# Kernel optimization log

Measured on AMD Instinct MI355X. Metric: run time of the kernel, lower is better.

Reference implementation:

```python
import jax, jax.numpy as jnp
import numpy as np

N_TICKS = 550
N_PMTS = 12
SI = 47  # SiPM grid is 47x47 = 2209
BIN_SIGMA = 0.1
GAUSS_NORM = 1.0 / (BIN_SIGMA * 2.5066282746)


def _dense_init(k, fan_in, fan_out):
    lim = float(np.sqrt(6.0 / (fan_in + fan_out)))  # glorot_uniform (keras Dense default)
    W = jax.random.uniform(k, (fan_in, fan_out), jnp.float32, -lim, lim)
    b = jnp.zeros((fan_out,), jnp.float32)
    return W, b


def setup_inputs() -> dict:
    key = jax.random.key(0)
    ks = jax.random.split(key, 10)
    B, N = 4, 8192  # events x electrons-per-event (ragged list densified)
    xy = jax.random.normal(ks[0], (B, N, 2), jnp.float32)
    z = jax.random.uniform(ks[1], (B, N, 1), jnp.float32, minval=0.0, maxval=549.0)
    electrons = jnp.concatenate([xy, z], axis=-1)  # [B, N, 3] = (x, y, z_ticks)
    weight = jax.random.uniform(ks[2], (B, N), jnp.float32)  # lifetime survival weight
    Wp1, bp1 = _dense_init(ks[3], 2, 28)
    Wp2, bp2 = _dense_init(ks[4], 28, N_PMTS)
    Ws1, bs1 = _dense_init(ks[5], 2, 64)
    Ws2, bs2 = _dense_init(ks[6], 64, 128)
    Ws3, bs3 = _dense_init(ks[7], 128, 256)
    Ws4, bs4 = _dense_init(ks[8], 256, SI * SI)
    pmt_scale = jnp.ones((N_PMTS,), jnp.float32)
    si_scale = jnp.ones((SI * SI,), jnp.float32)
    return dict(electrons=electrons, weight=weight,
                Wp1=Wp1, bp1=bp1, Wp2=Wp2, bp2=bp2, pmt_scale=pmt_scale,
                Ws1=Ws1, bs1=bs1, Ws2=Ws2, bs2=bs2, Ws3=Ws3, bs3=bs3,
                Ws4=Ws4, bs4=bs4, si_scale=si_scale)


def reference(electrons, weight, Wp1, bp1, Wp2, bp2, pmt_scale,
              Ws1, bs1, Ws2, bs2, Ws3, bs3, Ws4, bs4, si_scale):
    B = electrons.shape[0]
    xy = electrons[..., 0:2]            # [B, N, 2]
    z = electrons[..., 2]               # [B, N] in tick units
    # tf.linspace(0.5, n_ticks-0.5, 550) == bin centers
    ticks = jnp.arange(N_TICKS, dtype=electrons.dtype) + 0.5  # [T]
    # per-electron Gaussian over time ticks, scaled by lifetime weight: [B, N, T]
    exp_values = (GAUSS_NORM
                  * jnp.exp(-(ticks - z[..., None]) ** 2 / BIN_SIGMA)
                  * weight[..., None])
    # PMT response MLP: 2 -> 28 -> 12, sigmoid activations
    h = jax.nn.sigmoid(xy @ Wp1 + bp1)
    pmt_resp = jax.nn.sigmoid(h @ Wp2 + bp2) * pmt_scale ** 2    # [B, N, 12]
    # sparse(hist)^T @ response, then transpose -> [B, 12, T]
    pmt_result = jnp.einsum('bnt,bnp->bpt', exp_values, pmt_resp)
    # SiPM response MLP: 2 -> 64 -> 128 -> 256 -> 2209, sigmoid activations
    s = jax.nn.sigmoid(xy @ Ws1 + bs1)
    s = jax.nn.sigmoid(s @ Ws2 + bs2)
    s = jax.nn.sigmoid(s @ Ws3 + bs3)
    sipm_resp = jax.nn.sigmoid(s @ Ws4 + bs4) * si_scale ** 2    # [B, N, 2209]
    sipm_result = jnp.einsum('bnt,bns->bst', exp_values, sipm_resp)  # [B, 2209, T]
    sipm_result = sipm_result.reshape(B, SI, SI, N_TICKS)
    return pmt_result, sipm_result
```

## Files before the change

kernel.cpp:

```cpp
#include <hip/hip_runtime.h>

typedef short short8 __attribute__((ext_vector_type(8)));
typedef short short4v __attribute__((ext_vector_type(4)));
typedef float f32x4 __attribute__((ext_vector_type(4)));

#define NT 550
#define NS 2209
#define NP 12
#define NBK 69
#define SC_NGRP 18
#define SC_GBK 4
#define SC_TW 32
#define NSG 139
#define GNRM 3.9894228040143f

typedef unsigned short bfu;

__device__ __forceinline__ bfu f2bf(float f) {
    unsigned int u = __float_as_uint(f);
    unsigned int r = (u + 0x7fffu + ((u >> 16) & 1u)) >> 16;
    return (bfu)r;
}

__device__ __forceinline__ float sigm(float x) {
    return __builtin_amdgcn_rcpf(1.0f + __expf(-x));
}

__global__ void k_prep(const float* __restrict__ W2, const float* __restrict__ W3,
                       const float* __restrict__ W4,
                       bfu* __restrict__ w2h, bfu* __restrict__ w3h, bfu* __restrict__ w4h) {
    int id = blockIdx.x * 256 + threadIdx.x;
    if (id < 8192) {
        int c = id >> 6, k = id & 63;
        w2h[id] = f2bf(W2[k * 128 + c]);
    } else if (id < 8192 + 32768) {
        int j = id - 8192;
        int c = j >> 7, k = j & 127;
        w3h[j] = f2bf(W3[k * 256 + c]);
    } else {
        int j = id - 40960;
        int s = j >> 8, k = j & 255;
        w4h[j] = f2bf(s < NS ? W4[k * NS + s] : 0.0f);
    }
}

__global__ void k_count(const float* __restrict__ el, int* __restrict__ counts) {
    int id = blockIdx.x * 256 + threadIdx.x;
    float z = el[id * 3 + 2];
    int bk = (int)(z * 0.125f);
    bk = bk < 0 ? 0 : (bk > NBK - 1 ? NBK - 1 : bk);
    atomicAdd(&counts[(id >> 13) * NBK + bk], 1);
}

__global__ void k_scan(const int* __restrict__ counts, int* __restrict__ offs) {
    __shared__ int a[512];
    int tid = threadIdx.x;
    int v = (tid < 4 * NBK) ? counts[tid] : 0;
    a[tid] = v;
    __syncthreads();
    for (int s = 1; s < 512; s <<= 1) {
        int t = (tid >= s) ? a[tid - s] : 0;
        __syncthreads();
        a[tid] += t;
        __syncthreads();
    }
    if (tid < 4 * NBK) offs[tid] = a[tid] - v;
}

__global__ void k_scatter(const float* __restrict__ el, const float* __restrict__ wt,
                          const int* __restrict__ offs, int* __restrict__ cur,
                          int* __restrict__ inv, float4* __restrict__ elp) {
    int id = blockIdx.x * 256 + threadIdx.x;
    float x = el[id * 3], y = el[id * 3 + 1], z = el[id * 3 + 2];
    int bk = (int)(z * 0.125f);
    bk = bk < 0 ? 0 : (bk > NBK - 1 ? NBK - 1 : bk);
    int key = (id >> 13) * NBK + bk;
    int pos = offs[key] + atomicAdd(&cur[key], 1);
    inv[id] = pos;
    elp[pos] = make_float4(x, y, z, wt[id]);
}

__global__ __launch_bounds__(256, 1) void k_mlp(
    const float* __restrict__ el,
    const float* __restrict__ Ws1, const float* __restrict__ bs1,
    const float* __restrict__ bs2, const float* __restrict__ bs3,
    const bfu* __restrict__ w2h, const bfu* __restrict__ w3h,
    const int* __restrict__ inv, bfu* __restrict__ s3p) {

    __shared__ __align__(16) bfu bufA[32768];
    __shared__ __align__(16) bfu w3t[32768];
    __shared__ float xyb[256];
    __shared__ float s1w[128];
    __shared__ float b1s[64], b2s[128], b3s[256];

    bfu* h1t = bufA;
    bfu* w2t = bufA + 8192;
    bfu* h2t = bufA + 16384;

    const int tid = threadIdx.x;
    const int wv = tid >> 6, ln = tid & 63;
    const int e0 = blockIdx.x * 128;

    if (tid < 128) s1w[tid] = Ws1[tid];
    if (tid < 64) b1s[tid] = bs1[tid];
    if (tid < 128) b2s[tid] = bs2[tid];
    b3s[tid] = bs3[tid];

    if (tid < 128) {
        int e = e0 + tid;
        xyb[tid * 2] = el[e * 3]; xyb[tid * 2 + 1] = el[e * 3 + 1];
    }
    for (int i = 0; i < 4; ++i) {
        int cid = i * 256 + tid;
        int row = cid >> 3, c5 = cid & 7;
        short8 v = *(const short8*)(const void*)&w2h[row * 64 + c5 * 8];
        *(short8*)(void*)&w2t[row * 64 + ((c5 ^ (row & 7)) * 8)] = v;
    }
    for (int i = 0; i < 16; ++i) {
        int cid = i * 256 + tid;
        int row = cid >> 4, c5 = cid & 15;
        short8 v = *(const short8*)(const void*)&w3h[row * 128 + c5 * 8];
        *(short8*)(void*)&w3t[row * 128 + ((c5 ^ (row & 7)) * 8)] = v;
    }
    __syncthreads();

    {
        int n = tid & 127;
        int j0 = (tid >> 7) * 32;
        float xx = xyb[n * 2], yy = xyb[n * 2 + 1];
        for (int jj = 0; jj < 32; ++jj) {
            int j = j0 + jj;
            float h = sigm(xx * s1w[j] + yy * s1w[64 + j] + b1s[j]);
            h1t[n * 64 + (((j >> 3) ^ (n & 7)) * 8) + (j & 7)] = f2bf(h);
        }
    }
    __syncthreads();

    {
        const int mr = (wv >> 1) * 64;
        const int nc = (wv & 1) * 64;
        f32x4 acc[4][4];
        for (int m = 0; m < 4; ++m) for (int nf = 0; nf < 4; ++nf) acc[m][nf] = (f32x4){0.f, 0.f, 0.f, 0.f};
        for (int kk = 0; kk < 2; ++kk) {
            int kc = kk * 4 + (ln >> 4);
            short8 af[4], bf[4];
            for (int m = 0; m < 4; ++m) {
                int row = mr + 16 * m + (ln & 15);
                af[m] = *(const short8*)(const void*)&h1t[row * 64 + ((kc ^ (row & 7)) * 8)];
            }
            for (int nf = 0; nf < 4; ++nf) {
                int c = nc + 16 * nf + (ln & 15);
                bf[nf] = *(const short8*)(const void*)&w2t[c * 64 + ((kc ^ (c & 7)) * 8)];
            }
            for (int m = 0; m < 4; ++m)
                for (int nf = 0; nf < 4; ++nf)
                    acc[m][nf] = __builtin_amdgcn_mfma_f32_16x16x32_bf16(af[m], bf[nf], acc[m][nf], 0, 0, 0);
        }
        for (int m = 0; m < 4; ++m)
            for (int nf = 0; nf < 4; ++nf) {
                int c = nc + 16 * nf + (ln & 15);
                float bb = b2s[c];
                for (int r = 0; r < 4; ++r) {
                    int n = mr + 16 * m + (ln >> 4) * 4 + r;
                    float hh = sigm(acc[m][nf][r] + bb);
                    h2t[n * 128 + (((c >> 3) ^ (n & 7)) * 8) + (c & 7)] = f2bf(hh);
                }
            }
    }
    __syncthreads();

    f32x4 acc3[4][8];
    const int mr3 = (wv >> 1) * 64;
    const int nc3 = (wv & 1) * 128;
    for (int m = 0; m < 4; ++m) for (int nf = 0; nf < 8; ++nf) acc3[m][nf] = (f32x4){0.f, 0.f, 0.f, 0.f};
    for (int kk = 0; kk < 4; ++kk) {
        int kc = kk * 4 + (ln >> 4);
        short8 af[4];
        for (int m = 0; m < 4; ++m) {
            int row = mr3 + 16 * m + (ln & 15);
            af[m] = *(const short8*)(const void*)&h2t[row * 128 + ((kc ^ (row & 7)) * 8)];
        }
        for (int nf = 0; nf < 8; ++nf) {
            int c = nc3 + 16 * nf + (ln & 15);
            short8 bf = *(const short8*)(const void*)&w3t[c * 128 + ((kc ^ (c & 7)) * 8)];
            for (int m = 0; m < 4; ++m)
                acc3[m][nf] = __builtin_amdgcn_mfma_f32_16x16x32_bf16(af[m], bf, acc3[m][nf], 0, 0, 0);
        }
    }
    __syncthreads();
    for (int m = 0; m < 4; ++m)
        for (int nf = 0; nf < 8; ++nf) {
            int c = nc3 + 16 * nf + (ln & 15);
            float bb = b3s[c];
            for (int r = 0; r < 4; ++r) {
                int n = mr3 + 16 * m + (ln >> 4) * 4 + r;
                float ss = sigm(acc3[m][nf][r] + bb);
                bufA[n * 256 + (((c >> 3) ^ (n & 7)) * 8) + (c & 7)] = f2bf(ss);
            }
        }
    __syncthreads();
    for (int i = 0; i < 16; ++i) {
        int cid = i * 256 + tid;
        int row = cid >> 5, c5 = cid & 31;
        short8 v = *(const short8*)(const void*)&bufA[row * 256 + ((c5 ^ (row & 7)) * 8)];
        int dst = inv[e0 + row];
        *(short8*)(void*)&s3p[(size_t)dst * 256 + c5 * 8] = v;
    }
}

__global__ __launch_bounds__(512, 2) void k_g1(
    const float* __restrict__ bs4, const float* __restrict__ sis,
    const bfu* __restrict__ s3p, const bfu* __restrict__ w4h,
    bfu* __restrict__ resp) {

    __shared__ __align__(16) bfu s3t[2][64 * 256];

    const int tid = threadIdx.x;
    const int wv = tid >> 6, ln = tid & 63;
    const int st = blockIdx.x >> 5;
    const int cg = blockIdx.x & 31;
    const int s0 = st * 128;
    const int wn2 = (wv & 1) * 32;
    const int wsg = (wv >> 1) * 32;
    const int slot00 = cg * 1024;

    short8 bfr[2][8];
    float bssr[2], si2r[2];
#pragma unroll
    for (int nf = 0; nf < 2; ++nf) {
        int scol = s0 + wsg + 16 * nf + (ln & 15);
        const bfu* wp = &w4h[(size_t)scol * 256 + (ln >> 4) * 8];
#pragma unroll
        for (int kk = 0; kk < 8; ++kk)
            bfr[nf][kk] = *(const short8*)(const void*)&wp[kk * 32];
        bssr[nf] = (scol < NS) ? bs4[scol] : 0.0f;
        float sc = (scol < NS) ? sis[scol] : 0.0f;
        si2r[nf] = sc * sc;
    }

    const int rowS = tid >> 3;
    const int gq = tid & 7;
    const int r3 = rowS & 7;
    short8 rg0, rg1, rg2, rg3;

    auto ISSUE = [&](int c) {
        const bfu* p = s3p + ((size_t)(slot00 + c * 64 + rowS)) * 256 + gq * 8;
        rg0 = *(const short8*)(const void*)&p[0];
        rg1 = *(const short8*)(const void*)&p[64];
        rg2 = *(const short8*)(const void*)&p[128];
        rg3 = *(const short8*)(const void*)&p[192];
    };
    auto WSTAGE = [&](int buf) {
        bfu* drow = s3t[buf] + rowS * 256;
        *(short8*)(void*)&drow[(((0 * 8 + gq) ^ r3) * 8)] = rg0;
        *(short8*)(void*)&drow[(((1 * 8 + gq) ^ r3) * 8)] = rg1;
        *(short8*)(void*)&drow[(((2 * 8 + gq) ^ r3) * 8)] = rg2;
        *(short8*)(void*)&drow[(((3 * 8 + gq) ^ r3) * 8)] = rg3;
    };

    ISSUE(0); WSTAGE(0);
    __syncthreads();

    for (int c = 0; c < 16; ++c) {
        if (c + 1 < 16) ISSUE(c + 1);

        const bfu* sb = s3t[c & 1];
        f32x4 acc00 = (f32x4){0.f,0.f,0.f,0.f};
        f32x4 acc01 = (f32x4){0.f,0.f,0.f,0.f};
        f32x4 acc10 = (f32x4){0.f,0.f,0.f,0.f};
        f32x4 acc11 = (f32x4){0.f,0.f,0.f,0.f};
        const int ar0 = wn2 + (ln & 15), ar1 = wn2 + 16 + (ln & 15);
#pragma unroll
        for (int kk = 0; kk < 8; ++kk) {
            int kc = kk * 4 + (ln >> 4);
            short8 a0 = *(const short8*)(const void*)&sb[ar0 * 256 + ((kc ^ (ar0 & 7)) * 8)];
            short8 a1 = *(const short8*)(const void*)&sb[ar1 * 256 + ((kc ^ (ar1 & 7)) * 8)];
            acc00 = __builtin_amdgcn_mfma_f32_16x16x32_bf16(a0, bfr[0][kk], acc00, 0, 0, 0);
            acc01 = __builtin_amdgcn_mfma_f32_16x16x32_bf16(a0, bfr[1][kk], acc01, 0, 0, 0);
            acc10 = __builtin_amdgcn_mfma_f32_16x16x32_bf16(a1, bfr[0][kk], acc10, 0, 0, 0);
            acc11 = __builtin_amdgcn_mfma_f32_16x16x32_bf16(a1, bfr[1][kk], acc11, 0, 0, 0);
        }
        if (c + 1 < 16) WSTAGE((c + 1) & 1);

        {
            int sc0 = s0 + wsg + (ln & 15);
            int sc1 = sc0 + 16;
            int base = slot00 + c * 64;
            int n0a = base + wn2 + (ln >> 4) * 4;
            int n0b = n0a + 16;
            short4v pk;
#pragma unroll
            for (int r = 0; r < 4; ++r) pk[r] = (short)f2bf(si2r[0] * sigm(acc00[r] + bssr[0]));
            *(short4v*)(void*)&resp[(size_t)sc0 * 32768 + n0a] = pk;
#pragma unroll
            for (int r = 0; r < 4; ++r) pk[r] = (short)f2bf(si2r[1] * sigm(acc01[r] + bssr[1]));
            *(short4v*)(void*)&resp[(size_t)sc1 * 32768 + n0a] = pk;
#pragma unroll
            for (int r = 0; r < 4; ++r) pk[r] = (short)f2bf(si2r[0] * sigm(acc10[r] + bssr[0]));
            *(short4v*)(void*)&resp[(size_t)sc0 * 32768 + n0b] = pk;
#pragma unroll
            for (int r = 0; r < 4; ++r) pk[r] = (short)f2bf(si2r[1] * sigm(acc11[r] + bssr[1]));
            *(short4v*)(void*)&resp[(size_t)sc1 * 32768 + n0b] = pk;
        }
        __syncthreads();
    }
}

__global__ void k_egen(const float4* __restrict__ elp, bfu* __restrict__ Eg) {
    int slot = blockIdx.x * 256 + threadIdx.x;
    float4 e4 = elp[slot];
    int bk = (int)(e4.z * 0.125f);
    bk = bk < 0 ? 0 : (bk > NBK - 1 ? NBK - 1 : bk);
    float wG = e4.w * GNRM;
#pragma unroll
    for (int j = 0; j < 16; ++j) {
        int tg = bk * 8 - 4 + j;
        float d = (float)tg + 0.5f - e4.z;
        float g = (tg >= 0 && tg < NT) ? wG * __expf(-10.0f * d * d) : 0.0f;
        Eg[j * 32768 + slot] = f2bf(g);
    }
}

__global__ void k_pmtresp(const float* __restrict__ el, const int* __restrict__ inv,
                          const float* __restrict__ Wp1, const float* __restrict__ bp1,
                          const float* __restrict__ Wp2, const float* __restrict__ bp2,
                          const float* __restrict__ psc, bfu* __restrict__ resp) {
    int id = blockIdx.x * 256 + threadIdx.x;
    float x = el[id * 3], y = el[id * 3 + 1];
    float hh[28];
#pragma unroll
    for (int j = 0; j < 28; ++j)
        hh[j] = sigm(x * Wp1[j] + y * Wp1[28 + j] + bp1[j]);
    int dst = inv[id];
#pragma unroll
    for (int p = 0; p < 12; ++p) {
        float a = bp2[p];
#pragma unroll
        for (int j = 0; j < 28; ++j) a += hh[j] * Wp2[j * 12 + p];
        float sc = psc[p];
        resp[(size_t)(NS + p) * 32768 + dst] = f2bf(sigm(a) * sc * sc);
    }
}

__global__ __launch_bounds__(256, 4) void k_scat(
    const bfu* __restrict__ Eg, const bfu* __restrict__ resp,
    const int* __restrict__ counts, const int* __restrict__ offs,
    float* __restrict__ outP, float* __restrict__ outS) {

    __shared__ float ring[4 * 16 * 17];

    const int tid = threadIdx.x;
    const int ln = tid & 63, wv = tid >> 6;
    const int wid = blockIdx.x * 4 + wv;
    const int sgrp = wid % NSG;
    const int grp  = (wid / NSG) % SC_NGRP;
    const int b    = wid / (NSG * SC_NGRP);

    const int bk0 = grp * SC_GBK;
    const int bk1 = (bk0 + SC_GBK < NBK) ? bk0 + SC_GBK : NBK;
    const int T_lo = bk0 * 8 - 2;
    const int scol = sgrp * 16 + (ln & 15);
    const bfu* rrow = resp + (size_t)scol * 32768;
    const bfu* erow = Eg + (size_t)(ln & 15) * 32768;
    float* ringw = ring + wv * 272;

    for (int i = ln; i < 272; i += 64) ringw[i] = 0.f;

    int F = 0;
    for (int bk = (bk0 > 0 ? bk0 - 1 : 0); bk < bk1; ++bk) {
        const int cnt = counts[b * NBK + bk];
        if (cnt == 0) continue;
        const int off = offs[b * NBK + bk];
        const int db8 = (bk - bk0) * 8;

        {
            int Fn = db8 - 2; Fn = Fn < 0 ? 0 : Fn;
            for (int tl = F + (ln >> 4); tl < Fn; tl += 4) {
                float v = ringw[(tl & 15) * 17 + (ln & 15)];
                ringw[(tl & 15) * 17 + (ln & 15)] = 0.f;
                int tg = T_lo + tl;
                if (tg >= 0 && tg < NT) {
                    if (scol < NS)
                        outS[((size_t)b * NS + scol) * NT + tg] = v;
                    else if (scol < NS + NP)
                        outP[((size_t)b * NP + (scol - NS)) * NT + tg] = v;
                }
            }
            F = (Fn > F) ? Fn : F;
        }

        const int off0 = off & ~31;
        const int nks = (off + cnt - off0 + 31) >> 5;
        const int hi = off + cnt;
        f32x4 acc = (f32x4){0.f, 0.f, 0.f, 0.f};
        f32x4 acc1 = (f32x4){0.f, 0.f, 0.f, 0.f};
        int ks = 0;
        for (; ks + 1 < nks; ks += 2) {
            const int sb0 = off0 + ks * 32 + (ln >> 4) * 8;
            const int sb1 = sb0 + 32;
            short8 af0 = *(const short8*)(const void*)&erow[sb0];
            short8 af1 = *(const short8*)(const void*)&erow[sb1];
            short8 bb0 = *(const short8*)(const void*)&rrow[sb0];
            short8 bb1 = *(const short8*)(const void*)&rrow[sb1];
            if (ks == 0 && off0 < off) {
#pragma unroll
                for (int j = 0; j < 8; ++j) { int slot = sb0 + j; if (slot < off) af0[j] = 0; }
            }
            if (off0 + ks * 32 + 64 > hi) {
#pragma unroll
                for (int j = 0; j < 8; ++j) { int slot = sb0 + j; if (slot >= hi) af0[j] = 0; }
#pragma unroll
                for (int j = 0; j < 8; ++j) { int slot = sb1 + j; if (slot >= hi) af1[j] = 0; }
            }
            acc  = __builtin_amdgcn_mfma_f32_16x16x32_bf16(af0, bb0, acc, 0, 0, 0);
            acc1 = __builtin_amdgcn_mfma_f32_16x16x32_bf16(af1, bb1, acc1, 0, 0, 0);
        }
        if (ks < nks) {
            const int sb0 = off0 + ks * 32 + (ln >> 4) * 8;
            short8 af0 = *(const short8*)(const void*)&erow[sb0];
            short8 bb0 = *(const short8*)(const void*)&rrow[sb0];
            if ((ks == 0 && off0 < off) || (off0 + ks * 32 + 32 > hi)) {
#pragma unroll
                for (int j = 0; j < 8; ++j) {
                    int slot = sb0 + j;
                    if (slot < off || slot >= hi) af0[j] = 0;
                }
            }
            acc = __builtin_amdgcn_mfma_f32_16x16x32_bf16(af0, bb0, acc, 0, 0, 0);
        }

#pragma unroll
        for (int r = 0; r < 4; ++r) {
            int tl = db8 - 2 + (ln >> 4) * 4 + r;
            if (tl >= 0 && tl < SC_TW)
                ringw[(tl & 15) * 17 + (ln & 15)] += acc[r] + acc1[r];
        }
    }

    for (int tl = F + (ln >> 4); tl < SC_TW; tl += 4) {
        float v = ringw[(tl & 15) * 17 + (ln & 15)];
        int tg = T_lo + tl;
        if (tg >= 0 && tg < NT) {
            if (scol < NS)
                outS[((size_t)b * NS + scol) * NT + tg] = v;
            else if (scol < NS + NP)
                outP[((size_t)b * NP + (scol - NS)) * NT + tg] = v;
        }
    }
}

extern "C" void kernel_launch(void* const* d_in, const int* in_sizes, int n_in,
                              void* d_out, int out_size, void* d_ws, size_t ws_size,
                              hipStream_t stream) {
    const float* el  = (const float*)d_in[0];
    const float* wt  = (const float*)d_in[1];
    const float* Wp1 = (const float*)d_in[2];
    const float* bp1 = (const float*)d_in[3];
    const float* Wp2 = (const float*)d_in[4];
    const float* bp2 = (const float*)d_in[5];
    const float* psc = (const float*)d_in[6];
    const float* Ws1 = (const float*)d_in[7];
    const float* bs1 = (const float*)d_in[8];
    const float* Ws2 = (const float*)d_in[9];
    const float* bs2 = (const float*)d_in[10];
    const float* Ws3 = (const float*)d_in[11];
    const float* bs3 = (const float*)d_in[12];
    const float* Ws4 = (const float*)d_in[13];
    const float* bs4 = (const float*)d_in[14];
    const float* sis = (const float*)d_in[15];
    float* out = (float*)d_out;

    char* ws = (char*)d_ws;
    bfu* w2h     = (bfu*)(ws);
    bfu* w3h     = (bfu*)(ws + 16384);
    bfu* w4h     = (bfu*)(ws + 81920);
    bfu* Eg      = (bfu*)(ws + 81920);
    bfu* s3p     = (bfu*)(ws + 1261568);
    int* counts  = (int*)(ws + 18038784);
    int* offs    = (int*)(ws + 18042880);
    int* cursors = (int*)(ws + 18046976);
    int* inv     = (int*)(ws + 18051072);
    float4* elp  = (float4*)(ws + 18182144);
    bfu* resp    = (bfu*)(ws + 18706432);

    hipMemsetAsync(counts, 0, 4096, stream);
    hipMemsetAsync(cursors, 0, 4096, stream);

    k_prep<<<2464, 256, 0, stream>>>(Ws2, Ws3, Ws4, w2h, w3h, w4h);
    k_count<<<128, 256, 0, stream>>>(el, counts);
    k_scan<<<1, 512, 0, stream>>>(counts, offs);
    k_scatter<<<128, 256, 0, stream>>>(el, wt, offs, cursors, inv, elp);
    k_mlp<<<256, 256, 0, stream>>>(el, Ws1, bs1, bs2, bs3, w2h, w3h, inv, s3p);
    k_g1<<<18 * 32, 512, 0, stream>>>(bs4, sis, s3p, w4h, resp);
    k_egen<<<128, 256, 0, stream>>>(elp, Eg);
    k_pmtresp<<<128, 256, 0, stream>>>(el, inv, Wp1, bp1, Wp2, bp2, psc, resp);
    k_scat<<<(4 * SC_NGRP * NSG) / 4, 256, 0, stream>>>(Eg, resp, counts, offs,
                                                        out, out + 4 * NP * NT);
}
```

Measured before the change: 220.4 us.

## Drop LDS staging in SiPM final-layer GEMM, load A fragments directly per wave

The k_g1 GEMM no longer stages activation tiles through double-buffered shared memory with block barriers. Each wave now owns a 32-column by 64-row tile and loads its MFMA A fragments straight from global memory, with four independent 64-row chunks per wave and 4608 waves launched in 256-thread blocks. The aim is to remove LDS traffic and __syncthreads stalls and to raise occupancy. The cost is that waves covering different column groups reread the same activation rows from global memory or L2, with less coalesced 16-byte loads.

```diff
diff --git a/kernel.cpp b/kernel.cpp
--- a/kernel.cpp
+++ b/kernel.cpp
@@ -208,101 +208,103 @@
     }
 }
 
-__global__ __launch_bounds__(512, 2) void k_g1(
+__global__ __launch_bounds__(256, 4) void k_g1(
     const float* __restrict__ bs4, const float* __restrict__ sis,
     const bfu* __restrict__ s3p, const bfu* __restrict__ w4h,
     bfu* __restrict__ resp) {
 
-    __shared__ __align__(16) bfu s3t[2][64 * 256];
-
     const int tid = threadIdx.x;
-    const int wv = tid >> 6, ln = tid & 63;
-    const int st = blockIdx.x >> 5;
-    const int cg = blockIdx.x & 31;
+    const int ln = tid & 63, wv = tid >> 6;
+    const int wid = blockIdx.x * 4 + wv;
+    const int cg = wid & 63;
+    const int wsgi = (wid >> 6) & 3;
+    const int st = wid >> 8;
     const int s0 = st * 128;
-    const int wn2 = (wv & 1) * 32;
-    const int wsg = (wv >> 1) * 32;
-    const int slot00 = cg * 1024;
-
-    short8 bfr[2][8];
-    float bssr[2], si2r[2];
-#pragma unroll
-    for (int nf = 0; nf < 2; ++nf) {
-        int scol = s0 + wsg + 16 * nf + (ln & 15);
-        const bfu* wp = &w4h[(size_t)scol * 256 + (ln >> 4) * 8];
-#pragma unroll
-        for (int kk = 0; kk < 8; ++kk)
-            bfr[nf][kk] = *(const short8*)(const void*)&wp[kk * 32];
-        bssr[nf] = (scol < NS) ? bs4[scol] : 0.0f;
-        float sc = (scol < NS) ? sis[scol] : 0.0f;
-        si2r[nf] = sc * sc;
-    }
-
-    const int rowS = tid >> 3;
-    const int gq = tid & 7;
-    const int r3 = rowS & 7;
-    short8 rg0, rg1, rg2, rg3;
-
-    auto ISSUE = [&](int c) {
-        const bfu* p = s3p + ((size_t)(slot00 + c * 64 + rowS)) * 256 + gq * 8;
-        rg0 = *(const short8*)(const void*)&p[0];
-        rg1 = *(const short8*)(const void*)&p[64];
-        rg2 = *(const short8*)(const void*)&p[128];
-        rg3 = *(const short8*)(const void*)&p[192];
-    };
-    auto WSTAGE = [&](int buf) {
-        bfu* drow = s3t[buf] + rowS * 256;
-        *(short8*)(void*)&drow[(((0 * 8 + gq) ^ r3) * 8)] = rg0;
-        *(short8*)(void*)&drow[(((1 * 8 + gq) ^ r3) * 8)] = rg1;
-        *(short8*)(void*)&drow[(((2 * 8 + gq) ^ r3) * 8)] = rg2;
-        *(short8*)(void*)&drow[(((3 * 8 + gq) ^ r3) * 8)] = rg3;
-    };
-
-    ISSUE(0); WSTAGE(0);
-    __syncthreads();
-
-    for (int c = 0; c < 16; ++c) {
-        if (c + 1 < 16) ISSUE(c + 1);
-
-        const bfu* sb = s3t[c & 1];
+    const int wsg = wsgi * 32;
+
+    short8 bfr0[8], bfr1[8];
+    float bssr0, bssr1, si2r0, si2r1;
+    {
+        int sc0 = s0 + wsg + (ln & 15);
+        int sc1 = sc0 + 16;
+        const bfu* wp0 = &w4h[(size_t)sc0 * 256 + (ln >> 4) * 8];
+        const bfu* wp1 = &w4h[(size_t)sc1 * 256 + (ln >> 4) * 8];
+#pragma unroll
+        for (int kk = 0; kk < 8; ++kk) {
+            bfr0[kk] = *(const short8*)(const void*)&wp0[kk * 32];
+            bfr1[kk] = *(const short8*)(const void*)&wp1[kk * 32];
+        }
+        bssr0 = (sc0 < NS) ? bs4[sc0] : 0.0f;
+        bssr1 = (sc1 < NS) ? bs4[sc1] : 0.0f;
+        float t0 = (sc0 < NS) ? sis[sc0] : 0.0f;
+        float t1 = (sc1 < NS) ? sis[sc1] : 0.0f;
+        si2r0 = t0 * t0;
+        si2r1 = t1 * t1;
+    }
+
+    const int sc0 = s0 + wsg + (ln & 15);
+    const int sc1 = sc0 + 16;
+    const int slot0 = cg * 512;
+    const int arow = ln & 15;
+    const int ko = (ln >> 4) * 8;
+
+    for (int c = 0; c < 8; ++c) {
+        const int sb = slot0 + c * 64;
         f32x4 acc00 = (f32x4){0.f,0.f,0.f,0.f};
         f32x4 acc01 = (f32x4){0.f,0.f,0.f,0.f};
         f32x4 acc10 = (f32x4){0.f,0.f,0.f,0.f};
         f32x4 acc11 = (f32x4){0.f,0.f,0.f,0.f};
-        const int ar0 = wn2 + (ln & 15), ar1 = wn2 + 16 + (ln & 15);
+        f32x4 acc20 = (f32x4){0.f,0.f,0.f,0.f};
+        f32x4 acc21 = (f32x4){0.f,0.f,0.f,0.f};
+        f32x4 acc30 = (f32x4){0.f,0.f,0.f,0.f};
+        f32x4 acc31 = (f32x4){0.f,0.f,0.f,0.f};
+        const bfu* a0p = &s3p[(size_t)(sb + arow) * 256 + ko];
+        const bfu* a1p = a0p + 16 * 256;
+        const bfu* a2p = a0p + 32 * 256;
+        const bfu* a3p = a0p + 48 * 256;
 #pragma unroll
         for (int kk = 0; kk < 8; ++kk) {
-            int kc = kk * 4 + (ln >> 4);
-            short8 a0 = *(const short8*)(const void*)&sb[ar0 * 256 + ((kc ^ (ar0 & 7)) * 8)];
-            short8 a1 = *(const short8*)(const void*)&sb[ar1 * 256 + ((kc ^ (ar1 & 7)) * 8)];
-            acc00 = __builtin_amdgcn_mfma_f32_16x16x32_bf16(a0, bfr[0][kk], acc00, 0, 0, 0);
-            acc01 = __builtin_amdgcn_mfma_f32_16x16x32_bf16(a0, bfr[1][kk], acc01, 0, 0, 0);
-            acc10 = __builtin_amdgcn_mfma_f32_16x16x32_bf16(a1, bfr[0][kk], acc10, 0, 0, 0);
-            acc11 = __builtin_amdgcn_mfma_f32_16x16x32_bf16(a1, bfr[1][kk], acc11, 0, 0, 0);
-        }
-        if (c + 1 < 16) WSTAGE((c + 1) & 1);
-
+            short8 am0 = *(const short8*)(const void*)&a0p[kk * 32];
+            short8 am1 = *(const short8*)(const void*)&a1p[kk * 32];
+            short8 am2 = *(const short8*)(const void*)&a2p[kk * 32];
+            short8 am3 = *(const short8*)(const void*)&a3p[kk * 32];
+            acc00 = __builtin_amdgcn_mfma_f32_16x16x32_bf16(am0, bfr0[kk], acc00, 0, 0, 0);
+            acc01 = __builtin_amdgcn_mfma_f32_16x16x32_bf16(am0, bfr1[kk], acc01, 0, 0, 0);
+            acc10 = __builtin_amdgcn_mfma_f32_16x16x32_bf16(am1, bfr0[kk], acc10, 0, 0, 0);
+            acc11 = __builtin_amdgcn_mfma_f32_16x16x32_bf16(am1, bfr1[kk], acc11, 0, 0, 0);
+            acc20 = __builtin_amdgcn_mfma_f32_16x16x32_bf16(am2, bfr0[kk], acc20, 0, 0, 0);
+            acc21 = __builtin_amdgcn_mfma_f32_16x16x32_bf16(am2, bfr1[kk], acc21, 0, 0, 0);
+            acc30 = __builtin_amdgcn_mfma_f32_16x16x32_bf16(am3, bfr0[kk], acc30, 0, 0, 0);
+            acc31 = __builtin_amdgcn_mfma_f32_16x16x32_bf16(am3, bfr1[kk], acc31, 0, 0, 0);
+        }
         {
-            int sc0 = s0 + wsg + (ln & 15);
-            int sc1 = sc0 + 16;
-            int base = slot00 + c * 64;
-            int n0a = base + wn2 + (ln >> 4) * 4;
-            int n0b = n0a + 16;
+            const int n0 = sb + (ln >> 4) * 4;
             short4v pk;
 #pragma unroll
-            for (int r = 0; r < 4; ++r) pk[r] = (short)f2bf(si2r[0] * sigm(acc00[r] + bssr[0]));
-            *(short4v*)(void*)&resp[(size_t)sc0 * 32768 + n0a] = pk;
-#pragma unroll
-            for (int r = 0; r < 4; ++r) pk[r] = (short)f2bf(si2r[1] * sigm(acc01[r] + bssr[1]));
-            *(short4v*)(void*)&resp[(size_t)sc1 * 32768 + n0a] = pk;
-#pragma unroll
-            for (int r = 0; r < 4; ++r) pk[r] = (short)f2bf(si2r[0] * sigm(acc10[r] + bssr[0]));
-            *(short4v*)(void*)&resp[(size_t)sc0 * 32768 + n0b] = pk;
-#pragma unroll
-            for (int r = 0; r < 4; ++r) pk[r] = (short)f2bf(si2r[1] * sigm(acc11[r] + bssr[1]));
-            *(short4v*)(void*)&resp[(size_t)sc1 * 32768 + n0b] = pk;
-        }
-        __syncthreads();
+            for (int r = 0; r < 4; ++r) pk[r] = (short)f2bf(si2r0 * sigm(acc00[r] + bssr0));
+            *(short4v*)(void*)&resp[(size_t)sc0 * 32768 + n0] = pk;
+#pragma unroll
+            for (int r = 0; r < 4; ++r) pk[r] = (short)f2bf(si2r1 * sigm(acc01[r] + bssr1));
+            *(short4v*)(void*)&resp[(size_t)sc1 * 32768 + n0] = pk;
+#pragma unroll
+            for (int r = 0; r < 4; ++r) pk[r] = (short)f2bf(si2r0 * sigm(acc10[r] + bssr0));
+            *(short4v*)(void*)&resp[(size_t)sc0 * 32768 + n0 + 16] = pk;
+#pragma unroll
+            for (int r = 0; r < 4; ++r) pk[r] = (short)f2bf(si2r1 * sigm(acc11[r] + bssr1));
+            *(short4v*)(void*)&resp[(size_t)sc1 * 32768 + n0 + 16] = pk;
+#pragma unroll
+            for (int r = 0; r < 4; ++r) pk[r] = (short)f2bf(si2r0 * sigm(acc20[r] + bssr0));
+            *(short4v*)(void*)&resp[(size_t)sc0 * 32768 + n0 + 32] = pk;
+#pragma unroll
+            for (int r = 0; r < 4; ++r) pk[r] = (short)f2bf(si2r1 * sigm(acc21[r] + bssr1));
+            *(short4v*)(void*)&resp[(size_t)sc1 * 32768 + n0 + 32] = pk;
+#pragma unroll
+            for (int r = 0; r < 4; ++r) pk[r] = (short)f2bf(si2r0 * sigm(acc30[r] + bssr0));
+            *(short4v*)(void*)&resp[(size_t)sc0 * 32768 + n0 + 48] = pk;
+#pragma unroll
+            for (int r = 0; r < 4; ++r) pk[r] = (short)f2bf(si2r1 * sigm(acc31[r] + bssr1));
+            *(short4v*)(void*)&resp[(size_t)sc1 * 32768 + n0 + 48] = pk;
+        }
     }
 }
 
@@ -491,7 +493,7 @@
     k_scan<<<1, 512, 0, stream>>>(counts, offs);
     k_scatter<<<128, 256, 0, stream>>>(el, wt, offs, cursors, inv, elp);
     k_mlp<<<256, 256, 0, stream>>>(el, Ws1, bs1, bs2, bs3, w2h, w3h, inv, s3p);
-    k_g1<<<18 * 32, 512, 0, stream>>>(bs4, sis, s3p, w4h, resp);
+    k_g1<<<4608 / 4, 256, 0, stream>>>(bs4, sis, s3p, w4h, resp);
     k_egen<<<128, 256, 0, stream>>>(elp, Eg);
     k_pmtresp<<<128, 256, 0, stream>>>(el, inv, Wp1, bp1, Wp2, bp2, psc, resp);
     k_scat<<<(4 * SC_NGRP * NSG) / 4, 256, 0, stream>>>(Eg, resp, counts, offs,
```

After: 336.4 us. 1.53x slower.

## Reuse staged activation tiles across three SiPM column tiles in k_g1

Applied to the files above, without the earlier changes.

The final SiPM layer GEMM kernel now has each block cover 512 electron slots across three 128-column SiPM tiles, instead of 1024 slots for a single column tile. Each staged 64-row activation chunk in shared memory is reused for three weight tiles. This cuts the re-reading of s3p from global memory, with 384 blocks launched instead of 576. In exchange, the W4 weight fragments are reloaded from global memory on every chunk and tile instead of being held in registers, which adds load latency inside the loop.

```diff
diff --git a/kernel.cpp b/kernel.cpp
--- a/kernel.cpp
+++ b/kernel.cpp
@@ -217,26 +217,11 @@
 
     const int tid = threadIdx.x;
     const int wv = tid >> 6, ln = tid & 63;
-    const int st = blockIdx.x >> 5;
-    const int cg = blockIdx.x & 31;
-    const int s0 = st * 128;
+    const int stg = blockIdx.x >> 6;
+    const int cg  = blockIdx.x & 63;
     const int wn2 = (wv & 1) * 32;
     const int wsg = (wv >> 1) * 32;
-    const int slot00 = cg * 1024;
-
-    short8 bfr[2][8];
-    float bssr[2], si2r[2];
-#pragma unroll
-    for (int nf = 0; nf < 2; ++nf) {
-        int scol = s0 + wsg + 16 * nf + (ln & 15);
-        const bfu* wp = &w4h[(size_t)scol * 256 + (ln >> 4) * 8];
-#pragma unroll
-        for (int kk = 0; kk < 8; ++kk)
-            bfr[nf][kk] = *(const short8*)(const void*)&wp[kk * 32];
-        bssr[nf] = (scol < NS) ? bs4[scol] : 0.0f;
-        float sc = (scol < NS) ? sis[scol] : 0.0f;
-        si2r[nf] = sc * sc;
-    }
+    const int slot00 = cg * 512;
 
     const int rowS = tid >> 3;
     const int gq = tid & 7;
@@ -261,47 +246,67 @@
     ISSUE(0); WSTAGE(0);
     __syncthreads();
 
-    for (int c = 0; c < 16; ++c) {
-        if (c + 1 < 16) ISSUE(c + 1);
+    for (int c = 0; c < 8; ++c) {
+        if (c + 1 < 8) ISSUE(c + 1);
 
         const bfu* sb = s3t[c & 1];
-        f32x4 acc00 = (f32x4){0.f,0.f,0.f,0.f};
-        f32x4 acc01 = (f32x4){0.f,0.f,0.f,0.f};
-        f32x4 acc10 = (f32x4){0.f,0.f,0.f,0.f};
-        f32x4 acc11 = (f32x4){0.f,0.f,0.f,0.f};
         const int ar0 = wn2 + (ln & 15), ar1 = wn2 + 16 + (ln & 15);
-#pragma unroll
-        for (int kk = 0; kk < 8; ++kk) {
-            int kc = kk * 4 + (ln >> 4);
-            short8 a0 = *(const short8*)(const void*)&sb[ar0 * 256 + ((kc ^ (ar0 & 7)) * 8)];
-            short8 a1 = *(const short8*)(const void*)&sb[ar1 * 256 + ((kc ^ (ar1 & 7)) * 8)];
-            acc00 = __builtin_amdgcn_mfma_f32_16x16x32_bf16(a0, bfr[0][kk], acc00, 0, 0, 0);
-            acc01 = __builtin_amdgcn_mfma_f32_16x16x32_bf16(a0, bfr[1][kk], acc01, 0, 0, 0);
-            acc10 = __builtin_amdgcn_mfma_f32_16x16x32_bf16(a1, bfr[0][kk], acc10, 0, 0, 0);
-            acc11 = __builtin_amdgcn_mfma_f32_16x16x32_bf16(a1, bfr[1][kk], acc11, 0, 0, 0);
-        }
-        if (c + 1 < 16) WSTAGE((c + 1) & 1);
-
-        {
-            int sc0 = s0 + wsg + (ln & 15);
-            int sc1 = sc0 + 16;
-            int base = slot00 + c * 64;
-            int n0a = base + wn2 + (ln >> 4) * 4;
-            int n0b = n0a + 16;
-            short4v pk;
-#pragma unroll
-            for (int r = 0; r < 4; ++r) pk[r] = (short)f2bf(si2r[0] * sigm(acc00[r] + bssr[0]));
-            *(short4v*)(void*)&resp[(size_t)sc0 * 32768 + n0a] = pk;
-#pragma unroll
-            for (int r = 0; r < 4; ++r) pk[r] = (short)f2bf(si2r[1] * sigm(acc01[r] + bssr[1]));
-            *(short4v*)(void*)&resp[(size_t)sc1 * 32768 + n0a] = pk;
-#pragma unroll
-            for (int r = 0; r < 4; ++r) pk[r] = (short)f2bf(si2r[0] * sigm(acc10[r] + bssr[0]));
-            *(short4v*)(void*)&resp[(size_t)sc0 * 32768 + n0b] = pk;
-#pragma unroll
-            for (int r = 0; r < 4; ++r) pk[r] = (short)f2bf(si2r[1] * sigm(acc11[r] + bssr[1]));
-            *(short4v*)(void*)&resp[(size_t)sc1 * 32768 + n0b] = pk;
-        }
+        const int base = slot00 + c * 64;
+        const int n0a = base + wn2 + (ln >> 4) * 4;
+        const int n0b = n0a + 16;
+
+#pragma unroll
+        for (int q = 0; q < 3; ++q) {
+            const int stq = stg * 3 + q;
+            const int s0 = stq * 128;
+            const int sc0 = s0 + wsg + (ln & 15);
+            const int sc1 = sc0 + 16;
+            short8 bfr0[8], bfr1[8];
+            const bfu* wp0 = &w4h[(size_t)sc0 * 256 + (ln >> 4) * 8];
+            const bfu* wp1 = &w4h[(size_t)sc1 * 256 + (ln >> 4) * 8];
+#pragma unroll
+            for (int kk = 0; kk < 8; ++kk) {
+                bfr0[kk] = *(const short8*)(const void*)&wp0[kk * 32];
+                bfr1[kk] = *(const short8*)(const void*)&wp1[kk * 32];
+            }
+            float bssr0 = (sc0 < NS) ? bs4[sc0] : 0.0f;
+            float bssr1 = (sc1 < NS) ? bs4[sc1] : 0.0f;
+            float t0 = (sc0 < NS) ? sis[sc0] : 0.0f;
+            float t1 = (sc1 < NS) ? sis[sc1] : 0.0f;
+            float si2r0 = t0 * t0, si2r1 = t1 * t1;
+
+            f32x4 acc00 = (f32x4){0.f,0.f,0.f,0.f};
+            f32x4 acc01 = (f32x4){0.f,0.f,0.f,0.f};
+            f32x4 acc10 = (f32x4){0.f,0.f,0.f,0.f};
+            f32x4 acc11 = (f32x4){0.f,0.f,0.f,0.f};
+#pragma unroll
+            for (int kk = 0; kk < 8; ++kk) {
+                int kc = kk * 4 + (ln >> 4);
+                short8 a0 = *(const short8*)(const void*)&sb[ar0 * 256 + ((kc ^ (ar0 & 7)) * 8)];
+                short8 a1 = *(const short8*)(const void*)&sb[ar1 * 256 + ((kc ^ (ar1 & 7)) * 8)];
+                acc00 = __builtin_amdgcn_mfma_f32_16x16x32_bf16(a0, bfr0[kk], acc00, 0, 0, 0);
+                acc01 = __builtin_amdgcn_mfma_f32_16x16x32_bf16(a0, bfr1[kk], acc01, 0, 0, 0);
+                acc10 = __builtin_amdgcn_mfma_f32_16x16x32_bf16(a1, bfr0[kk], acc10, 0, 0, 0);
+                acc11 = __builtin_amdgcn_mfma_f32_16x16x32_bf16(a1, bfr1[kk], acc11, 0, 0, 0);
+            }
+            {
+                short4v pk;
+#pragma unroll
+                for (int r = 0; r < 4; ++r) pk[r] = (short)f2bf(si2r0 * sigm(acc00[r] + bssr0));
+                *(short4v*)(void*)&resp[(size_t)sc0 * 32768 + n0a] = pk;
+#pragma unroll
+                for (int r = 0; r < 4; ++r) pk[r] = (short)f2bf(si2r1 * sigm(acc01[r] + bssr1));
+                *(short4v*)(void*)&resp[(size_t)sc1 * 32768 + n0a] = pk;
+#pragma unroll
+                for (int r = 0; r < 4; ++r) pk[r] = (short)f2bf(si2r0 * sigm(acc10[r] + bssr0));
+                *(short4v*)(void*)&resp[(size_t)sc0 * 32768 + n0b] = pk;
+#pragma unroll
+                for (int r = 0; r < 4; ++r) pk[r] = (short)f2bf(si2r1 * sigm(acc11[r] + bssr1));
+                *(short4v*)(void*)&resp[(size_t)sc1 * 32768 + n0b] = pk;
+            }
+        }
+
+        if (c + 1 < 8) WSTAGE((c + 1) & 1);
         __syncthreads();
     }
 }
@@ -491,7 +496,7 @@
     k_scan<<<1, 512, 0, stream>>>(counts, offs);
     k_scatter<<<128, 256, 0, stream>>>(el, wt, offs, cursors, inv, elp);
     k_mlp<<<256, 256, 0, stream>>>(el, Ws1, bs1, bs2, bs3, w2h, w3h, inv, s3p);
-    k_g1<<<18 * 32, 512, 0, stream>>>(bs4, sis, s3p, w4h, resp);
+    k_g1<<<384, 512, 0, stream>>>(bs4, sis, s3p, w4h, resp);
     k_egen<<<128, 256, 0, stream>>>(elp, Eg);
     k_pmtresp<<<128, 256, 0, stream>>>(el, inv, Wp1, bp1, Wp2, bp2, psc, resp);
     k_scat<<<(4 * SC_NGRP * NSG) / 4, 256, 0, stream>>>(Eg, resp, counts, offs,
```

Measured after the change: 370.2 us. 1.68x slower.
